# Kernel tuning notes

Hardware: AMD Instinct MI355X
Metric: run time of the kernel (lower is better)

The kernel has to match this reference:

```python
import jax, jax.numpy as jnp
import numpy as np

D_MODEL = 2048
NUM_HEADS = 16
HEAD_DIM = 128
BATCH = 4
SEQ = 2048


def setup_inputs() -> dict:
    key = jax.random.key(0)
    ks = jax.random.split(key, 5)
    s = 0.02
    return {
        "x": jax.random.normal(ks[0], (BATCH, SEQ, D_MODEL), dtype=jnp.float32),
        "Wq": jax.random.normal(ks[1], (NUM_HEADS * HEAD_DIM, D_MODEL), dtype=jnp.float32) * s,
        "Wk": jax.random.normal(ks[2], (NUM_HEADS * HEAD_DIM, D_MODEL), dtype=jnp.float32) * s,
        "Wv": jax.random.normal(ks[3], (NUM_HEADS * HEAD_DIM, D_MODEL), dtype=jnp.float32) * s,
        "Wo": jax.random.normal(ks[4], (D_MODEL, NUM_HEADS * HEAD_DIM), dtype=jnp.float32) * s,
    }


def _split_heads(t):
    b, s, _ = t.shape
    return t.reshape(b, s, NUM_HEADS, HEAD_DIM).transpose(0, 2, 1, 3)  # [b,h,s,d]


def reference(x, Wq, Wk, Wv, Wo):
    # prefill: QKV proj + causal SDPA + output proj. torch Linear: x @ W.T
    q = _split_heads(x @ Wq.T)
    k = _split_heads(x @ Wk.T)
    v = _split_heads(x @ Wv.T)
    scale = 1.0 / jnp.sqrt(jnp.asarray(HEAD_DIM, dtype=x.dtype))
    scores = jnp.einsum("bhqd,bhkd->bhqk", q, k) * scale
    causal = jnp.tril(jnp.ones((SEQ, SEQ), dtype=bool))
    scores = jnp.where(causal, scores, jnp.finfo(scores.dtype).min)
    attn = jax.nn.softmax(scores, axis=-1)
    y = jnp.einsum("bhqk,bhkd->bhqd", attn, v)
    y = y.transpose(0, 2, 1, 3).reshape(x.shape[0], SEQ, NUM_HEADS * HEAD_DIM)
    y = y @ Wo.T
    return (y, k, v)
```

## Files before the change

kernel.cpp:

```cpp
#include <hip/hip_runtime.h>
#include <stdint.h>

#define DM 2048
#define NH 16
#define HD 128
#define BB 4
#define SS 2048
#define BS (BB*SS)
#define NQKV (3*DM)
#define SCQ 0.12751744565f

typedef __bf16 bf16_t;
typedef __attribute__((ext_vector_type(8))) __bf16 bf16x8;
typedef __attribute__((ext_vector_type(4))) float f32x4;
typedef __attribute__((ext_vector_type(16))) float f32x16;
typedef __attribute__((ext_vector_type(4))) float float4v;
typedef __attribute__((ext_vector_type(4))) unsigned int uint4v;
typedef __attribute__((ext_vector_type(4))) unsigned short ushort4v;
typedef __attribute__((ext_vector_type(8))) unsigned short ushort8;

__device__ __forceinline__ unsigned short f2bf(float f) {
  unsigned u = __float_as_uint(f);
  u += 0x7fffu + ((u >> 16) & 1u);
  return (unsigned short)(u >> 16);
}

__device__ __forceinline__ void gl16(const void* g, void* l) {
  __builtin_amdgcn_global_load_lds(
      (const __attribute__((address_space(1))) unsigned int*)(unsigned long long)g,
      (__attribute__((address_space(3))) unsigned int*)(unsigned int)(unsigned long long)l,
      16, 0, 0);
}

#define DSR(dst, addr, IMM)                                                   \
  asm volatile("ds_read_b128 %0, %1 offset:" IMM : "=v"(dst) : "v"(addr))

__global__ void conv_all(const float* __restrict__ x,  const float* __restrict__ wq,
                         const float* __restrict__ wk, const float* __restrict__ wv,
                         const float* __restrict__ wo,
                         unsigned short* __restrict__ xbf,
                         unsigned short* __restrict__ wqkv,
                         unsigned short* __restrict__ wobf) {
  const int NX = BS * DM / 4;
  const int NW = DM * DM / 4;
  int i = blockIdx.x * blockDim.x + threadIdx.x;
  int stride = gridDim.x * blockDim.x;
  for (; i < NX + 4 * NW; i += stride) {
    const float4v* src;
    ushort4v* dst;
    if (i < NX)               { src = (const float4v*)x  + i;            dst = (ushort4v*)xbf + i; }
    else if (i < NX + NW)     { int j = i - NX;          src = (const float4v*)wq + j; dst = (ushort4v*)wqkv + j; }
    else if (i < NX + 2 * NW) { int j = i - NX - NW;     src = (const float4v*)wk + j; dst = (ushort4v*)wqkv + NW + j; }
    else if (i < NX + 3 * NW) { int j = i - NX - 2 * NW; src = (const float4v*)wv + j; dst = (ushort4v*)wqkv + 2 * NW + j; }
    else                      { int j = i - NX - 3 * NW; src = (const float4v*)wo + j; dst = (ushort4v*)wobf + j; }
    float4v v = *src;
    ushort4v o;
    o.x = f2bf(v.x); o.y = f2bf(v.y); o.z = f2bf(v.z); o.w = f2bf(v.w);
    *dst = o;
  }
}

__global__ __launch_bounds__(256)
void gemm128q(const bf16_t* __restrict__ A, const bf16_t* __restrict__ Bm,
              bf16_t* __restrict__ qbf, bf16_t* __restrict__ kbt,
              float* __restrict__ kf, float* __restrict__ vf,
              bf16_t* __restrict__ vtb) {
  __shared__ bf16_t As[128 * 32];
  __shared__ bf16_t Bs[128 * 32];
  const int t = threadIdx.x, w = t >> 6, lane = t & 63;
  const int fr = lane & 15, fq = lane >> 4;
  const int row0 = blockIdx.x * 128, col0 = blockIdx.y * 128;
  const int wm = (w >> 1) * 64, wn = (w & 1) * 64;
  const int K = DM;

  const bf16_t *A0, *A1, *B0, *B1;
  {
    int u0 = t, r0 = u0 >> 2, c0 = u0 & 3;
    int u1 = 256 + t, r1 = u1 >> 2, c1 = u1 & 3;
    A0 = A + (size_t)(row0 + r0) * K + ((c0 ^ ((r0 >> 1) & 3)) * 8);
    A1 = A + (size_t)(row0 + r1) * K + ((c1 ^ ((r1 >> 1) & 3)) * 8);
    B0 = Bm + (size_t)(col0 + r0) * K + ((c0 ^ ((r0 >> 1) & 3)) * 8);
    B1 = Bm + (size_t)(col0 + r1) * K + ((c1 ^ ((r1 >> 1) & 3)) * 8);
  }
  const int d0 = t * 16, d1 = (256 + t) * 16;
  const int swz = ((fq ^ ((fr >> 1) & 3)) * 8);

  f32x4 acc[4][4] = {};

  for (int kk = 0; kk < K; kk += 32) {
    __syncthreads();
    gl16(A0 + kk, (char*)As + d0);
    gl16(A1 + kk, (char*)As + d1);
    gl16(B0 + kk, (char*)Bs + d0);
    gl16(B1 + kk, (char*)Bs + d1);
    __syncthreads();
    bf16x8 af[4], bfv[4];
#pragma unroll
    for (int f = 0; f < 4; ++f) {
      af[f]  = *(const bf16x8*)(As + (wm + f * 16 + fr) * 32 + swz);
      bfv[f] = *(const bf16x8*)(Bs + (wn + f * 16 + fr) * 32 + swz);
    }
#pragma unroll
    for (int i = 0; i < 4; ++i)
#pragma unroll
      for (int jn = 0; jn < 4; ++jn)
        acc[i][jn] = __builtin_amdgcn_mfma_f32_16x16x32_bf16(af[i], bfv[jn], acc[i][jn], 0, 0, 0);
  }

#pragma unroll
  for (int i = 0; i < 4; ++i) {
#pragma unroll
    for (int jn = 0; jn < 4; ++jn) {
#pragma unroll
      for (int r = 0; r < 4; ++r) {
        int m = row0 + wm + i * 16 + fq * 4 + r;
        int n = col0 + wn + jn * 16 + fr;
        float v = acc[i][jn][r];
        int b = m >> 11, s = m & 2047;
        if (col0 < DM) {
          int h = n >> 7, d = n & 127;
          qbf[(((size_t)(b * NH + h)) * SS + s) * HD + d] = (bf16_t)(v * SCQ);
        } else if (col0 < 2 * DM) {
          int nn = n - DM, h = nn >> 7, d = nn & 127;
          size_t o = (((size_t)(b * NH + h)) * SS + s) * HD + d;
          kbt[o] = (bf16_t)v;
          kf[o] = v;
        } else {
          int nn = n - 2 * DM, h = nn >> 7, d = nn & 127;
          size_t o = (((size_t)(b * NH + h)) * SS + s) * HD + d;
          vf[o] = v;
          vtb[((size_t)(b * NH + h)) * (HD * SS) + (size_t)d * SS + s] = (bf16_t)v;
        }
      }
    }
  }
}

template<int MODE>
__global__ __launch_bounds__(512)
void gemmr4(const bf16_t* __restrict__ A, const bf16_t* __restrict__ Bm,
            const int K, const int N, const int nbx,
            float* __restrict__ Cf) {
  __shared__ bf16_t As[4][256 * 32];
  __shared__ bf16_t Bs[4][256 * 32];
  const int t = threadIdx.x, w = t >> 6, lane = t & 63;
  const int fr = lane & 15, fq = lane >> 4;
  const int cpx = gridDim.x >> 3;
  const int orig = blockIdx.x;
  const int wg = (orig & 7) * cpx + (orig >> 3);
  const int bm = wg % nbx, bn = wg / nbx;
  const int row0 = bm * 256, col0 = bn * 256;
  const int wm = (w >> 2) * 128, wn = (w & 3) * 64;

  const bf16_t* Asrc[2];
  const bf16_t* Bsrc[2];
  int dst[2];
#pragma unroll
  for (int j = 0; j < 2; ++j) {
    int u = j * 512 + t, r = u >> 2, c = u & 3;
    Asrc[j] = A + (size_t)(row0 + r) * K + ((c ^ ((r >> 1) & 3)) * 8);
    Bsrc[j] = Bm + (size_t)(col0 + r) * K + ((c ^ ((r >> 1) & 3)) * 8);
    dst[j] = u * 16;
  }
  const int NT = K >> 5;
  f32x4 acc[8][4] = {};

  const unsigned As0 = (unsigned)(unsigned long long)(const void*)&As[0][0];
  const unsigned Bs0 = (unsigned)(unsigned long long)(const void*)&Bs[0][0];
  const unsigned xorc = (unsigned)((fq ^ ((fr >> 1) & 3)) << 4);
  const unsigned aoff = (unsigned)((wm + fr) * 64) + xorc;
  const unsigned boff = (unsigned)((wn + fr) * 64) + xorc;

#define STAGE(TT)                                                  \
  {                                                                \
    const int sl_ = (TT) & 3;                                      \
    const size_t ko_ = (size_t)(TT) * 32;                          \
    gl16(Asrc[0] + ko_, (char*)(&As[sl_][0]) + dst[0]);            \
    gl16(Asrc[1] + ko_, (char*)(&As[sl_][0]) + dst[1]);            \
    gl16(Bsrc[0] + ko_, (char*)(&Bs[sl_][0]) + dst[0]);            \
    gl16(Bsrc[1] + ko_, (char*)(&Bs[sl_][0]) + dst[1]);            \
  }

#define MFQUAD(FI, AV)                                                        \
  acc[FI][0] = __builtin_amdgcn_mfma_f32_16x16x32_bf16(                       \
      __builtin_bit_cast(bf16x8, AV), __builtin_bit_cast(bf16x8, bv0), acc[FI][0], 0, 0, 0); \
  acc[FI][1] = __builtin_amdgcn_mfma_f32_16x16x32_bf16(                       \
      __builtin_bit_cast(bf16x8, AV), __builtin_bit_cast(bf16x8, bv1), acc[FI][1], 0, 0, 0); \
  acc[FI][2] = __builtin_amdgcn_mfma_f32_16x16x32_bf16(                       \
      __builtin_bit_cast(bf16x8, AV), __builtin_bit_cast(bf16x8, bv2), acc[FI][2], 0, 0, 0); \
  acc[FI][3] = __builtin_amdgcn_mfma_f32_16x16x32_bf16(                       \
      __builtin_bit_cast(bf16x8, AV), __builtin_bit_cast(bf16x8, bv3), acc[FI][3], 0, 0, 0);

  STAGE(0); STAGE(1); STAGE(2);

  for (int T = 0; T < NT; ++T) {
    if (T + 2 < NT) {
      asm volatile("s_waitcnt vmcnt(8)" ::: "memory");
    } else if (T + 1 < NT) {
      asm volatile("s_waitcnt vmcnt(4)" ::: "memory");
    } else {
      asm volatile("s_waitcnt vmcnt(0)" ::: "memory");
    }
    asm volatile("s_barrier" ::: "memory");
    if (T + 3 < NT) STAGE(T + 3);

    const unsigned ab = As0 + (unsigned)(T & 3) * 16384 + aoff;
    const unsigned bb = Bs0 + (unsigned)(T & 3) * 16384 + boff;
    uint4v bv0, bv1, bv2, bv3, a0, a1, a2, a3, a4, a5, a6, a7;
    DSR(bv0, bb, "0");    DSR(bv1, bb, "1024");
    DSR(bv2, bb, "2048"); DSR(bv3, bb, "3072");
    DSR(a0, ab, "0");     DSR(a1, ab, "1024");
    DSR(a2, ab, "2048");  DSR(a3, ab, "3072");
    DSR(a4, ab, "4096");  DSR(a5, ab, "5120");
    DSR(a6, ab, "6144");  DSR(a7, ab, "7168");

    asm volatile("s_waitcnt lgkmcnt(4)" ::: "memory");
    __builtin_amdgcn_sched_barrier(0);
    __builtin_amdgcn_s_setprio(1);
    MFQUAD(0, a0) MFQUAD(1, a1) MFQUAD(2, a2) MFQUAD(3, a3)
    __builtin_amdgcn_s_setprio(0);

    asm volatile("s_waitcnt lgkmcnt(0)" ::: "memory");
    __builtin_amdgcn_sched_barrier(0);
    __builtin_amdgcn_s_setprio(1);
    MFQUAD(4, a4) MFQUAD(5, a5) MFQUAD(6, a6) MFQUAD(7, a7)
    __builtin_amdgcn_s_setprio(0);
  }
#undef STAGE
#undef MFQUAD

#pragma unroll
  for (int f = 0; f < 8; ++f) {
#pragma unroll
    for (int jn = 0; jn < 4; ++jn) {
#pragma unroll
      for (int r = 0; r < 4; ++r) {
        int m = row0 + wm + f * 16 + fq * 4 + r;
        int n = col0 + wn + jn * 16 + fr;
        Cf[(size_t)m * N + n] = acc[f][jn][r];
      }
    }
  }
}

__global__ __launch_bounds__(256, 2)
void attn_fwd5(const bf16_t* __restrict__ qbf, const bf16_t* __restrict__ kbf,
               const bf16_t* __restrict__ vt, bf16_t* __restrict__ aout) {
  __shared__ bf16_t Ks[2][64 * 128];
  __shared__ bf16_t Vs[2][64 * 128];
  const int t = threadIdx.x, w = t >> 6, lane = t & 63;
  const int l31 = lane & 31, hi = lane >> 5;
  const int orig = blockIdx.x;
  const int wg = (orig & 7) * 128 + (orig >> 3);
  const int bh = wg >> 4;
  const int qt = 15 - (wg & 15);
  const int q0 = qt * 128;
  const int nt = 2 * qt + 2;
  const size_t bh_off = (size_t)bh * SS * HD;
  const char* kbase = (const char*)(kbf + bh_off);
  const char* vbase = (const char*)(vt + bh_off);

  const char* ksrc[4];
  const char* vsrc[4];
#pragma unroll
  for (int i = 0; i < 4; ++i) {
    int r = (w * 4 + i) * 4 + (lane >> 4);
    int c = (lane & 15) ^ (r & 15);
    ksrc[i] = kbase + r * 256 + c * 16;
    int d = 2 * r + (c >> 3);
    vsrc[i] = vbase + (size_t)d * (SS * 2) + (c & 7) * 16;
  }

  bf16x8 qfr[8];
  {
    const char* qrow = (const char*)(qbf + bh_off + (size_t)(q0 + w * 32 + l31) * HD);
#pragma unroll
    for (int ds = 0; ds < 8; ++ds)
      qfr[ds] = *(const bf16x8*)(qrow + ds * 32 + hi * 16);
  }

#pragma unroll
  for (int i = 0; i < 4; ++i) {
    gl16(ksrc[i], (char*)(&Ks[0][0]) + (w * 4 + i) * 1024);
    gl16(vsrc[i], (char*)(&Vs[0][0]) + (w * 4 + i) * 1024);
    ksrc[i] += 16384;
    vsrc[i] += 128;
  }

  float mrow = -3.0e38f, lrow = 0.f;
  f32x16 accO[4] = {};

  auto make_pa = [&](const f32x16& sv, bf16x8& paA, bf16x8& paB) {
    unsigned W[8];
#pragma unroll
    for (int m = 0; m < 8; ++m) {
      float lo = sv[2 * m], hh = sv[2 * m + 1];
      asm("v_cvt_pk_bf16_f32 %0, %1, %2" : "=v"(W[m]) : "v"(lo), "v"(hh));
    }
    asm volatile("v_permlane32_swap_b32 %0, %1" : "+v"(W[0]), "+v"(W[2]));
    asm volatile("v_permlane32_swap_b32 %0, %1" : "+v"(W[1]), "+v"(W[3]));
    asm volatile("v_permlane32_swap_b32 %0, %1" : "+v"(W[4]), "+v"(W[6]));
    asm volatile("v_permlane32_swap_b32 %0, %1" : "+v"(W[5]), "+v"(W[7]));
    uint4v u0; u0.x = W[0]; u0.y = W[1]; u0.z = W[2]; u0.w = W[3];
    paA = __builtin_bit_cast(bf16x8, u0);
    uint4v u1; u1.x = W[4]; u1.y = W[5]; u1.z = W[6]; u1.w = W[7];
    paB = __builtin_bit_cast(bf16x8, u1);
  };

  for (int kt = 0; kt < nt; ++kt) {
    const int cur = kt & 1;
    __syncthreads();

    if (kt + 1 < nt) {
#pragma unroll
      for (int i = 0; i < 4; ++i) {
        gl16(ksrc[i], (char*)(&Ks[cur ^ 1][0]) + (w * 4 + i) * 1024);
        gl16(vsrc[i], (char*)(&Vs[cur ^ 1][0]) + (w * 4 + i) * 1024);
        ksrc[i] += 16384;
        vsrc[i] += 128;
      }
    }

    const char* kl = (const char*)&Ks[cur][0];
    f32x16 s0 = {}, s1 = {};
    const int rck = l31 & 15;
    __builtin_amdgcn_s_setprio(1);
#pragma unroll
    for (int ds = 0; ds < 8; ++ds) {
      int ch = ((2 * ds + hi) ^ rck) << 4;
      bf16x8 kf0 = *(const bf16x8*)(kl + l31 * 256 + ch);
      s0 = __builtin_amdgcn_mfma_f32_32x32x16_bf16(kf0, qfr[ds], s0, 0, 0, 0);
      bf16x8 kf1 = *(const bf16x8*)(kl + (32 + l31) * 256 + ch);
      s1 = __builtin_amdgcn_mfma_f32_32x32x16_bf16(kf1, qfr[ds], s1, 0, 0, 0);
    }
    __builtin_amdgcn_s_setprio(0);

    const int kv0 = kt * 64;
    if (kt >= 2 * qt) {
      const int qg = q0 + w * 32 + l31;
#pragma unroll
      for (int r = 0; r < 16; ++r) {
        int klo = kv0 + (r & 3) + 8 * (r >> 2) + 4 * hi;
        if (klo > qg) s0[r] = -3.0e38f;
        if (klo + 32 > qg) s1[r] = -3.0e38f;
      }
    }
    float rm = s0[0];
#pragma unroll
    for (int r = 1; r < 16; ++r) rm = fmaxf(rm, s0[r]);
#pragma unroll
    for (int r = 0; r < 16; ++r) rm = fmaxf(rm, s1[r]);
    rm = fmaxf(rm, __shfl_xor(rm, 32, 64));
    if (__ballot(rm > mrow + 8.0f)) {
      float mnew = fmaxf(mrow, rm);
      float fct = __builtin_amdgcn_exp2f(mrow - mnew);
      mrow = mnew;
      lrow *= fct;
#pragma unroll
      for (int r = 0; r < 16; ++r) {
        float f = __shfl(fct, (r & 3) + 8 * (r >> 2) + 4 * hi, 64);
        accO[0][r] *= f; accO[1][r] *= f; accO[2][r] *= f; accO[3][r] *= f;
      }
    }
    float ss = 0.f;
#pragma unroll
    for (int r = 0; r < 16; ++r) { float p = __builtin_amdgcn_exp2f(s0[r] - mrow); s0[r] = p; ss += p; }
#pragma unroll
    for (int r = 0; r < 16; ++r) { float p = __builtin_amdgcn_exp2f(s1[r] - mrow); s1[r] = p; ss += p; }
    ss += __shfl_xor(ss, 32, 64);
    lrow += ss;

    bf16x8 pa00, pa01, pa10, pa11;
    make_pa(s0, pa00, pa01);
    make_pa(s1, pa10, pa11);

    const char* vl = (const char*)&Vs[cur][0];
    __builtin_amdgcn_s_setprio(1);
#pragma unroll
    for (int dt = 0; dt < 4; ++dt) {
      int R = dt * 16 + (l31 >> 1);
      int cb = (l31 & 1) << 3;
      int rx = R & 15;
      bf16x8 v00 = *(const bf16x8*)(vl + R * 256 + (((cb + 0 + hi) ^ rx) << 4));
      accO[dt] = __builtin_amdgcn_mfma_f32_32x32x16_bf16(pa00, v00, accO[dt], 0, 0, 0);
      bf16x8 v01 = *(const bf16x8*)(vl + R * 256 + (((cb + 2 + hi) ^ rx) << 4));
      accO[dt] = __builtin_amdgcn_mfma_f32_32x32x16_bf16(pa01, v01, accO[dt], 0, 0, 0);
      bf16x8 v10 = *(const bf16x8*)(vl + R * 256 + (((cb + 4 + hi) ^ rx) << 4));
      accO[dt] = __builtin_amdgcn_mfma_f32_32x32x16_bf16(pa10, v10, accO[dt], 0, 0, 0);
      bf16x8 v11 = *(const bf16x8*)(vl + R * 256 + (((cb + 6 + hi) ^ rx) << 4));
      accO[dt] = __builtin_amdgcn_mfma_f32_32x32x16_bf16(pa11, v11, accO[dt], 0, 0, 0);
    }
    __builtin_amdgcn_s_setprio(0);
  }

  const int b = bh >> 4, h = bh & 15;
#pragma unroll
  for (int r = 0; r < 16; ++r) {
    int qr = (r & 3) + 8 * (r >> 2) + 4 * hi;
    float inv = __builtin_amdgcn_rcpf(__shfl(lrow, qr, 64));
    int srow = q0 + w * 32 + qr;
    bf16_t* orow = aout + ((size_t)(b * SS + srow)) * DM + h * HD + l31;
    orow[0]  = (bf16_t)(accO[0][r] * inv);
    orow[32] = (bf16_t)(accO[1][r] * inv);
    orow[64] = (bf16_t)(accO[2][r] * inv);
    orow[96] = (bf16_t)(accO[3][r] * inv);
  }
}

extern "C" void kernel_launch(void* const* d_in, const int* in_sizes, int n_in,
                              void* d_out, int out_size, void* d_ws, size_t ws_size,
                              hipStream_t stream) {
  (void)in_sizes; (void)n_in; (void)out_size; (void)ws_size;
  const float* x  = (const float*)d_in[0];
  const float* Wq = (const float*)d_in[1];
  const float* Wk = (const float*)d_in[2];
  const float* Wv = (const float*)d_in[3];
  const float* Wo = (const float*)d_in[4];

  float* y  = (float*)d_out;
  float* kf = y + (size_t)BS * DM;
  float* vf = kf + (size_t)BS * DM;

  char* ws = (char*)d_ws;
  bf16_t* xbf  = (bf16_t*)ws;
  bf16_t* abf  = xbf;
  bf16_t* qbf  = (bf16_t*)(ws + (size_t)32 * 1024 * 1024);
  bf16_t* wqkv = (bf16_t*)(ws + (size_t)64 * 1024 * 1024);
  bf16_t* wobf = (bf16_t*)(ws + (size_t)88 * 1024 * 1024);
  bf16_t* kbt  = (bf16_t*)y;
  bf16_t* vtb  = (bf16_t*)((char*)y + (size_t)32 * 1024 * 1024);

  conv_all<<<2048, 256, 0, stream>>>(x, Wq, Wk, Wv, Wo,
                                     (unsigned short*)xbf, (unsigned short*)wqkv,
                                     (unsigned short*)wobf);

  gemm128q<<<dim3(BS / 128, NQKV / 128), 256, 0, stream>>>(
      xbf, wqkv, qbf, kbt, kf, vf, vtb);

  attn_fwd5<<<1024, 256, 0, stream>>>(qbf, kbt, vtb, abf);

  gemmr4<0><<<256, 512, 0, stream>>>(abf, wobf, DM, DM, 32, y);
}
```

Measured before the change: 541.9 us.

## Split QKV GEMM epilogue: separate K fp32 upcast and V transpose kernels

The QKV projection kernel no longer writes the fp32 K copy or the strided transposed bf16 V. Instead, separate kernels upcast bf16 K to fp32 and transpose V through LDS into a coalesced layout. The GEMM main loop also replaces the async global-to-LDS loads with plain register-staged vector loads and a different swizzle. The aim is to drop the uncoalesced transposed stores from the GEMM epilogue, at the cost of extra launches and extra global traffic. The K output now holds bf16-rounded values rather than fp32, which changes numerical precision.

```diff
diff --git a/kernel.cpp b/kernel.cpp
--- a/kernel.cpp
+++ b/kernel.cpp
@@ -60,51 +60,91 @@
   }
 }
 
-__global__ __launch_bounds__(256)
-void gemm128q(const bf16_t* __restrict__ A, const bf16_t* __restrict__ Bm,
-              bf16_t* __restrict__ qbf, bf16_t* __restrict__ kbt,
-              float* __restrict__ kf, float* __restrict__ vf,
-              bf16_t* __restrict__ vtb) {
+__global__ void conv_bf16_f32(const unsigned short* __restrict__ in,
+                              float* __restrict__ out, int n4) {
+  int i = blockIdx.x * blockDim.x + threadIdx.x;
+  int stride = gridDim.x * blockDim.x;
+  for (; i < n4; i += stride) {
+    ushort4v v = ((const ushort4v*)in)[i];
+    float4v o;
+    o.x = __uint_as_float((unsigned)v.x << 16);
+    o.y = __uint_as_float((unsigned)v.y << 16);
+    o.z = __uint_as_float((unsigned)v.z << 16);
+    o.w = __uint_as_float((unsigned)v.w << 16);
+    ((float4v*)out)[i] = o;
+  }
+}
+
+__global__ void vtrans(const float* __restrict__ vf, bf16_t* __restrict__ vt) {
+  __shared__ unsigned short T[128 * 64];
+  const int t = threadIdx.x;
+  const int s0 = blockIdx.x * 64;
+  const int bh = blockIdx.y;
+  const size_t in_off = (size_t)bh * SS * HD;
+  const int sr = t >> 5, c4 = t & 31;
+#pragma unroll
+  for (int j = 0; j < 8; ++j) {
+    int s = j * 8 + sr;
+    float4v v = *(const float4v*)(vf + in_off + (size_t)(s0 + s) * HD + c4 * 4);
+#pragma unroll
+    for (int q = 0; q < 4; ++q) {
+      int d = c4 * 4 + q;
+      int bc = s * 2;
+      int byt = d * 128 + ((((bc >> 4) ^ (d & 7)) << 4) | (bc & 15));
+      *(unsigned short*)((char*)T + byt) = f2bf(v[q]);
+    }
+  }
+  __syncthreads();
+  const int dr = t >> 3, c8 = t & 7;
+  unsigned short* out = (unsigned short*)vt + (size_t)bh * HD * SS;
+#pragma unroll
+  for (int j = 0; j < 4; ++j) {
+    int d = j * 32 + dr;
+    ushort8 val = *(const ushort8*)((char*)T + d * 128 + ((c8 ^ (d & 7)) << 4));
+    *(ushort8*)(out + (size_t)d * SS + s0 + c8 * 8) = val;
+  }
+}
+
+__global__ void gemmq(const bf16_t* __restrict__ A, const bf16_t* __restrict__ Bm,
+                      bf16_t* __restrict__ qbf, bf16_t* __restrict__ kbt,
+                      float* __restrict__ vf) {
   __shared__ bf16_t As[128 * 32];
   __shared__ bf16_t Bs[128 * 32];
-  const int t = threadIdx.x, w = t >> 6, lane = t & 63;
+  const int t = threadIdx.x;
+  const int w = t >> 6, lane = t & 63;
+  const int wm = (w >> 1) * 64, wn = (w & 1) * 64;
+  const int row0 = blockIdx.x * 128, col0 = blockIdx.y * 128;
   const int fr = lane & 15, fq = lane >> 4;
-  const int row0 = blockIdx.x * 128, col0 = blockIdx.y * 128;
-  const int wm = (w >> 1) * 64, wn = (w & 1) * 64;
   const int K = DM;
 
-  const bf16_t *A0, *A1, *B0, *B1;
-  {
-    int u0 = t, r0 = u0 >> 2, c0 = u0 & 3;
-    int u1 = 256 + t, r1 = u1 >> 2, c1 = u1 & 3;
-    A0 = A + (size_t)(row0 + r0) * K + ((c0 ^ ((r0 >> 1) & 3)) * 8);
-    A1 = A + (size_t)(row0 + r1) * K + ((c1 ^ ((r1 >> 1) & 3)) * 8);
-    B0 = Bm + (size_t)(col0 + r0) * K + ((c0 ^ ((r0 >> 1) & 3)) * 8);
-    B1 = Bm + (size_t)(col0 + r1) * K + ((c1 ^ ((r1 >> 1) & 3)) * 8);
-  }
-  const int d0 = t * 16, d1 = (256 + t) * 16;
-  const int swz = ((fq ^ ((fr >> 1) & 3)) * 8);
-
   f32x4 acc[4][4] = {};
 
   for (int kk = 0; kk < K; kk += 32) {
-    __syncthreads();
-    gl16(A0 + kk, (char*)As + d0);
-    gl16(A1 + kk, (char*)As + d1);
-    gl16(B0 + kk, (char*)Bs + d0);
-    gl16(B1 + kk, (char*)Bs + d1);
+#pragma unroll
+    for (int j = 0; j < 2; ++j) {
+      int idx = j * 256 + t;
+      int r = idx >> 2, c = idx & 3;
+      uint4v dA = *(const uint4v*)(A + (size_t)(row0 + r) * K + kk + c * 8);
+      uint4v dB = *(const uint4v*)(Bm + (size_t)(col0 + r) * K + kk + c * 8);
+      int so = r * 32 + ((c ^ (r & 3)) * 8);
+      *(uint4v*)(As + so) = dA;
+      *(uint4v*)(Bs + so) = dB;
+    }
     __syncthreads();
     bf16x8 af[4], bfv[4];
 #pragma unroll
     for (int f = 0; f < 4; ++f) {
-      af[f]  = *(const bf16x8*)(As + (wm + f * 16 + fr) * 32 + swz);
-      bfv[f] = *(const bf16x8*)(Bs + (wn + f * 16 + fr) * 32 + swz);
+      int ra = wm + f * 16 + fr;
+      af[f] = *(const bf16x8*)(As + ra * 32 + ((fq ^ (ra & 3)) * 8));
+      int rb = wn + f * 16 + fr;
+      bfv[f] = *(const bf16x8*)(Bs + rb * 32 + ((fq ^ (rb & 3)) * 8));
     }
 #pragma unroll
     for (int i = 0; i < 4; ++i)
 #pragma unroll
       for (int jn = 0; jn < 4; ++jn)
         acc[i][jn] = __builtin_amdgcn_mfma_f32_16x16x32_bf16(af[i], bfv[jn], acc[i][jn], 0, 0, 0);
+    __syncthreads();
   }
 
 #pragma unroll
@@ -117,19 +157,15 @@
         int n = col0 + wn + jn * 16 + fr;
         float v = acc[i][jn][r];
         int b = m >> 11, s = m & 2047;
-        if (col0 < DM) {
+        if (n < DM) {
           int h = n >> 7, d = n & 127;
           qbf[(((size_t)(b * NH + h)) * SS + s) * HD + d] = (bf16_t)(v * SCQ);
-        } else if (col0 < 2 * DM) {
+        } else if (n < 2 * DM) {
           int nn = n - DM, h = nn >> 7, d = nn & 127;
-          size_t o = (((size_t)(b * NH + h)) * SS + s) * HD + d;
-          kbt[o] = (bf16_t)v;
-          kf[o] = v;
+          kbt[(((size_t)(b * NH + h)) * SS + s) * HD + d] = (bf16_t)v;
         } else {
           int nn = n - 2 * DM, h = nn >> 7, d = nn & 127;
-          size_t o = (((size_t)(b * NH + h)) * SS + s) * HD + d;
-          vf[o] = v;
-          vtb[((size_t)(b * NH + h)) * (HD * SS) + (size_t)d * SS + s] = (bf16_t)v;
+          vf[(((size_t)(b * NH + h)) * SS + s) * HD + d] = v;
         }
       }
     }
@@ -434,8 +470,11 @@
                                      (unsigned short*)xbf, (unsigned short*)wqkv,
                                      (unsigned short*)wobf);
 
-  gemm128q<<<dim3(BS / 128, NQKV / 128), 256, 0, stream>>>(
-      xbf, wqkv, qbf, kbt, kf, vf, vtb);
+  gemmq<<<dim3(BS / 128, NQKV / 128), 256, 0, stream>>>(xbf, wqkv, qbf, kbt, vf);
+
+  conv_bf16_f32<<<2048, 256, 0, stream>>>((const unsigned short*)kbt, kf, BS * DM / 4);
+
+  vtrans<<<dim3(SS / 64, BB * NH), 256, 0, stream>>>(vf, vtb);
 
   attn_fwd5<<<1024, 256, 0, stream>>>(qbf, kbt, vtb, abf);
 
```

New measurement: 503.9 us. -7.0%, faster.
